# Performance work log

Hardware: AMD Instinct MI355X
Metric: run time of the kernel (lower is better)

Reference implementation:

```python
import jax, jax.numpy as jnp
import numpy as np

EMBED_DIM = 1024
NUM_HEADS = 16
HEAD_DIM = EMBED_DIM // NUM_HEADS
B, T = 4, 1024
NEG = -1.0e9
LN_EPS = 1e-5


def setup_inputs() -> dict:
    key = jax.random.key(0)
    ks = jax.random.split(key, 13)
    s = 1.0 / np.sqrt(EMBED_DIM)
    return {
        "query": jax.random.normal(ks[0], (B, T, EMBED_DIM), jnp.float32),
        "key": jax.random.normal(ks[1], (B, T, EMBED_DIM), jnp.float32),
        "value": jax.random.normal(ks[2], (B, T, EMBED_DIM), jnp.float32),
        "mask": jax.random.randint(ks[3], (B, 1, T, T), 0, 2, jnp.int32),
        "Wq": jax.random.normal(ks[4], (EMBED_DIM, EMBED_DIM), jnp.float32) * s,
        "bq": jnp.zeros((EMBED_DIM,), jnp.float32),
        "Wk": jax.random.normal(ks[5], (EMBED_DIM, EMBED_DIM), jnp.float32) * s,
        "bk": jnp.zeros((EMBED_DIM,), jnp.float32),
        "Wv": jax.random.normal(ks[6], (EMBED_DIM, EMBED_DIM), jnp.float32) * s,
        "bv": jnp.zeros((EMBED_DIM,), jnp.float32),
        "Wo": jax.random.normal(ks[7], (EMBED_DIM, EMBED_DIM), jnp.float32) * s,
        "bo": jnp.zeros((EMBED_DIM,), jnp.float32),
        "gamma": jnp.ones((EMBED_DIM,), jnp.float32),
        "beta": jnp.zeros((EMBED_DIM,), jnp.float32),
    }


def _split_heads(x):
    # (B, T, E) -> (B, H, T, D)
    b, t, _ = x.shape
    return x.reshape(b, t, NUM_HEADS, HEAD_DIM).transpose(0, 2, 1, 3)


def _mha(query, key, value, mask, Wq, bq, Wk, bk, Wv, bv, Wo, bo, gamma, beta,
         temperature=1.0):
    q = _split_heads(query @ Wq.T + bq)
    k = _split_heads(key @ Wk.T + bk)
    v = _split_heads(value @ Wv.T + bv)
    # scores: (B, H, T, T)
    scale = jnp.sqrt(jnp.float32(HEAD_DIM)) * temperature
    scores = jnp.einsum("bhqd,bhkd->bhqk", q, k) / scale
    scores = jnp.where(mask == 0, NEG, scores)
    scores = scores - jnp.max(scores, axis=-1, keepdims=True)
    # temperature >= 0.01 in this config, so the low-temperature hard-cutoff
    # branch is skipped (matches torch's Python-level `if temperature < 0.01`).
    scores = jnp.nan_to_num(scores, nan=0.0, posinf=1.0e9, neginf=-1.0e9)
    attn = jax.nn.softmax(scores, axis=-1)
    # eval mode: dropout is identity (self.training is False)
    out = jnp.einsum("bhqk,bhkd->bhqd", attn, v)  # (B, H, T, D)
    out = out.transpose(0, 2, 1, 3).reshape(query.shape[0], query.shape[1], EMBED_DIM)
    out = out @ Wo.T + bo
    # layer norm over embed_dim
    mu = jnp.mean(out, axis=-1, keepdims=True)
    var = jnp.mean(jnp.square(out - mu), axis=-1, keepdims=True)
    out = (out - mu) * jax.lax.rsqrt(var + LN_EPS) * gamma + beta
    return out


def reference(query, key, value, mask, Wq, bq, Wk, bk, Wv, bv, Wo, bo, gamma, beta):
    return _mha(query, key, value, mask, Wq, bq, Wk, bk, Wv, bv, Wo, bo, gamma, beta)
```

## Files before the change

### kernel.cpp

```cpp
#include <hip/hip_runtime.h>
#include <cmath>

#define T_SEQ 1024
#define EMB   1024
#define NH    16
#define HD    64
#define NB    4
#define BQ    64
#define BK    64

#define QSCALE 0.18033688011112042f
#define BIAS2  -1.44269504e9f

using frag8   = __attribute__((ext_vector_type(8))) short;
using f32x4   = __attribute__((ext_vector_type(4))) float;
using short4v = __attribute__((ext_vector_type(4))) short;
using short8v = __attribute__((ext_vector_type(8))) short;

__device__ inline short f2bf(float f) {
    union { float f; unsigned u; } x; x.f = f;
    unsigned r = (x.u + 0x7FFFu + ((x.u >> 16) & 1u)) >> 16;
    return (short)r;
}
__device__ inline float bf2f(unsigned short u) {
    union { unsigned u; float f; } x; x.u = ((unsigned)u) << 16;
    return x.f;
}
__device__ inline int cvt_pk_bf16(float lo, float hi) {
    int r;
    asm("v_cvt_pk_bf16_f32 %0, %1, %2" : "=v"(r) : "v"(lo), "v"(hi));
    return r;
}

__device__ inline void glds16(const short* g, short* l) {
    __builtin_amdgcn_global_load_lds(
        (const __attribute__((address_space(1))) void*)g,
        (__attribute__((address_space(3))) void*)l, 16, 0, 0);
}

struct ConvArgs { const float* src[7]; short* dst[7]; int n8[7]; };

__global__ __launch_bounds__(256) void convert_bf16(ConvArgs a) {
    const int y = blockIdx.y;
    const int t = blockIdx.x * 256 + threadIdx.x;
    if (t >= a.n8[y]) return;
    const float4* s = (const float4*)a.src[y];
    const float4 v0 = s[t * 2], v1 = s[t * 2 + 1];
    short8v o;
    o[0] = f2bf(v0.x); o[1] = f2bf(v0.y); o[2] = f2bf(v0.z); o[3] = f2bf(v0.w);
    o[4] = f2bf(v1.x); o[5] = f2bf(v1.y); o[6] = f2bf(v1.z); o[7] = f2bf(v1.w);
    *(short8v*)&a.dst[y][t * 8] = o;
}

__global__ __launch_bounds__(256) void convert_mask(
    const int* __restrict__ mask, short* __restrict__ dst)
{
    const int wave = threadIdx.x >> 6, lane = threadIdx.x & 63;
    const int tile = blockIdx.x * 4 + wave;
    const int bb   = tile >> 12;
    const int q16  = (tile >> 6) & 63;
    const int k16  = tile & 63;
    const int qrow = lane >> 2;
    const int col4 = (lane & 3) * 4;
    const int4 mv = *(const int4*)&mask[((size_t)bb * T_SEQ + q16 * 16 + qrow) * T_SEQ
                                        + k16 * 16 + col4];
    const short BB = f2bf(BIAS2);
    short4v o;
    o[0] = mv.x ? (short)0 : BB;
    o[1] = mv.y ? (short)0 : BB;
    o[2] = mv.z ? (short)0 : BB;
    o[3] = mv.w ? (short)0 : BB;
    *(short4v*)&dst[(size_t)tile * 256 + qrow * 16 + col4] = o;
}

struct GemmB { const short* A; const short* W; const float* bias; short* out; float scale; };
struct QkvArgs { GemmB g[3]; };

template <int MODE>
__device__ inline void gemm_core(short* __restrict__ As,
                                 short* __restrict__ Bs,
                                 const short* __restrict__ A,
                                 const short* __restrict__ W,
                                 const float* __restrict__ bias,
                                 float scale,
                                 short* __restrict__ outS,
                                 float* __restrict__ outF,
                                 int m0, int n0)
{
    const int tid  = threadIdx.x;
    const int wave = tid >> 6;
    const int lane = tid & 63;
    const int quad = lane >> 4;
    const int lm   = lane & 15;
    const int wr   = wave >> 1;
    const int wc   = wave & 1;
    const int K    = EMB;

    const int G0 = wave * 64 + lane, G1 = G0 + 256;
    const short* aSrc0 = A + (size_t)(m0 + (G0 >> 2)) * K + (G0 & 3) * 8;
    const short* aSrc1 = A + (size_t)(m0 + (G1 >> 2)) * K + (G1 & 3) * 8;
    const short* bSrc0 = W + (size_t)(n0 + (G0 >> 2)) * K + (G0 & 3) * 8;
    const short* bSrc1 = W + (size_t)(n0 + (G1 >> 2)) * K + (G1 & 3) * 8;
    short* aDst0 = As + wave * 512;
    short* aDst1 = As + 2048 + wave * 512;
    short* bDst0 = Bs + wave * 512;
    short* bDst1 = Bs + 2048 + wave * 512;

    f32x4 acc[4][4];
#pragma unroll
    for (int i = 0; i < 4; ++i)
#pragma unroll
        for (int j = 0; j < 4; ++j) acc[i][j] = (f32x4){0.f, 0.f, 0.f, 0.f};

    for (int kk = 0; kk < K; kk += 64) {
        __syncthreads();
        glds16(aSrc0 + kk,      aDst0);
        glds16(aSrc1 + kk,      aDst1);
        glds16(bSrc0 + kk,      bDst0);
        glds16(bSrc1 + kk,      bDst1);
        glds16(aSrc0 + kk + 32, aDst0 + 4096);
        glds16(aSrc1 + kk + 32, aDst1 + 4096);
        glds16(bSrc0 + kk + 32, bDst0 + 4096);
        glds16(bSrc1 + kk + 32, bDst1 + 4096);
        __syncthreads();

#pragma unroll
        for (int p = 0; p < 2; ++p) {
            frag8 aF[4], bF[4];
#pragma unroll
            for (int i = 0; i < 4; ++i)
                aF[i] = *(const frag8*)&As[p * 4096 + (wr * 64 + i * 16 + lm) * 32 + quad * 8];
#pragma unroll
            for (int j = 0; j < 4; ++j)
                bF[j] = *(const frag8*)&Bs[p * 4096 + (wc * 64 + j * 16 + lm) * 32 + quad * 8];
#pragma unroll
            for (int i = 0; i < 4; ++i)
#pragma unroll
                for (int j = 0; j < 4; ++j)
                    acc[i][j] = __builtin_amdgcn_mfma_f32_16x16x32_bf16(
                        aF[i], bF[j], acc[i][j], 0, 0, 0);
        }
    }

#pragma unroll
    for (int i = 0; i < 4; ++i)
#pragma unroll
        for (int j = 0; j < 4; ++j) {
            const int n = n0 + wc * 64 + j * 16 + lm;
            const float bv = bias[n];
#pragma unroll
            for (int rr = 0; rr < 4; ++rr) {
                const int m = m0 + wr * 64 + i * 16 + quad * 4 + rr;
                const float val = (acc[i][j][rr] + bv) * scale;
                if (MODE == 0) {
                    outF[((size_t)(m >> 4) * 64 + (n >> 4)) * 256 +
                         rr * 64 + quad * 16 + lm] = val;
                } else {
                    const int bb = m >> 10, tt = m & 1023;
                    const int h = n >> 6,  d  = n & 63;
                    const size_t bh = (size_t)bb * NH + h;
                    if (MODE == 1) {
                        outS[((bh * 64 + (tt >> 4)) * 8 + (d >> 3)) * 128 +
                             (tt & 15) * 8 + (d & 7)] = f2bf(val);
                    } else {
                        outS[((((bh * 16 + (tt >> 6)) * 2 + ((tt >> 5) & 1)) * 4 +
                              (d >> 4)) * 4 + ((tt >> 2) & 3)) * 128 +
                             (d & 15) * 8 + (((tt & 16) >> 2) | (tt & 3))] = f2bf(val);
                    }
                }
            }
        }
}

__global__ __launch_bounds__(256, 4) void gemm_qkv(QkvArgs args) {
    __shared__ short As[2 * 128 * 32];
    __shared__ short Bs[2 * 128 * 32];
    const int id = blockIdx.x + 8 * blockIdx.y + 256 * blockIdx.z;
    const int a  = id & 7;
    const int k2 = id >> 3;
    const int nb = k2 & 7;
    const int c  = k2 >> 3;
    const int pair = a * 12 + c;
    const int mb = pair & 31;
    const int zb = pair >> 5;
    const GemmB g = args.g[zb];
    if (zb < 2) gemm_core<1>(As, Bs, g.A, g.W, g.bias, g.scale, g.out, nullptr, mb * 128, nb * 128);
    else        gemm_core<2>(As, Bs, g.A, g.W, g.bias, g.scale, g.out, nullptr, mb * 128, nb * 128);
}

__global__ __launch_bounds__(256, 4) void gemm_wo(const short* __restrict__ A,
                                                  const short* __restrict__ W,
                                                  const float* __restrict__ bias,
                                                  float* __restrict__ out) {
    __shared__ short As[2 * 128 * 32];
    __shared__ short Bs[2 * 128 * 32];
    const int id = blockIdx.x + 8 * blockIdx.y;
    const int a  = id & 7;
    const int k2 = id >> 3;
    const int nb = k2 & 7;
    const int c  = k2 >> 3;
    const int mb = a * 4 + c;
    gemm_core<0>(As, Bs, A, W, bias, 1.0f, nullptr, out, mb * 128, nb * 128);
}

__global__ __launch_bounds__(512, 4) void flash_attn_mfma(
    const short* __restrict__ qf_, const short* __restrict__ kf_,
    const short* __restrict__ vf_, const short* __restrict__ mf_,
    short* __restrict__ out)
{
    __shared__ short KV[2][4][4096];

    const int tid  = threadIdx.x;
    const int wave = tid >> 6;
    const int lane = tid & 63;
    const int quad = lane >> 4;
    const int lm   = lane & 15;
    const int wq   = wave & 3;
    const int wk   = wave >> 2;

    const int id  = blockIdx.x;
    const int xcd = id & 7;
    const int idx = id >> 3;
    const int bh_i = xcd * 8 + (idx >> 4);
    const int b  = bh_i >> 4, h = bh_i & 15;
    const int q0 = (idx & 15) * BQ;
    const size_t bh = (size_t)bh_i;

    const int  sbuf  = wave >> 1;
    const int  shalf = (wave & 1) * 2048;
    const short* sb = ((sbuf < 2) ? kf_ : vf_) + bh * 65536
                      + (size_t)(sbuf & 1) * 32768 + shalf + lane * 8;

    const short* qb_ = qf_ + (bh * 64 + (q0 >> 4) + wq) * 1024;
    const frag8 qfa = *(const frag8*)&qb_[(quad * 16 + lm) * 8];
    const frag8 qfb = *(const frag8*)&qb_[((quad + 4) * 16 + lm) * 8];

    const short* mrow = mf_ + ((size_t)b * 64 + (q0 >> 4) + wq) * (64 * 256)
                        + lm * 16 + quad * 4;

    union { int i[4]; frag8 f; } ones;
    ones.i[0] = ones.i[1] = ones.i[2] = ones.i[3] = 0x3F803F80;

    f32x4 of[4];
#pragma unroll
    for (int dc = 0; dc < 4; ++dc) of[dc] = (f32x4){0.f, 0.f, 0.f, 0.f};
    f32x4 ls = (f32x4){0.f, 0.f, 0.f, 0.f};

#pragma unroll
    for (int it = 0; it < 4; ++it)
        glds16(sb + it * 512, &KV[0][sbuf][shalf + it * 512]);
    short4v mb[4];
#pragma unroll
    for (int kc = 0; kc < 4; ++kc)
        mb[kc] = *(const short4v*)&mrow[(wk * 32 + kc) * 256];
    __syncthreads();

    for (int kt = 0; kt < 8; ++kt) {
        const int cur = kt & 1;

        if (kt < 7) {
#pragma unroll
            for (int it = 0; it < 4; ++it)
                glds16(sb + (kt + 1) * 4096 + it * 512,
                       &KV[cur ^ 1][sbuf][shalf + it * 512]);
        }
        short4v mc[4];
#pragma unroll
        for (int kc = 0; kc < 4; ++kc) mc[kc] = mb[kc];
        if (kt < 7) {
#pragma unroll
            for (int kc = 0; kc < 4; ++kc)
                mb[kc] = *(const short4v*)&mrow[((wk * 8 + kt + 1) * 4 + kc) * 256];
        }

        f32x4 s[4];
#pragma unroll
        for (int kc = 0; kc < 4; ++kc) {
            const short* kb = &KV[cur][wk][kc * 1024];
            const frag8 kfa = *(const frag8*)&kb[(quad * 16 + lm) * 8];
            const frag8 kfb = *(const frag8*)&kb[((quad + 4) * 16 + lm) * 8];
            f32x4 a = (f32x4){ bf2f((unsigned short)mc[kc][0]),
                               bf2f((unsigned short)mc[kc][1]),
                               bf2f((unsigned short)mc[kc][2]),
                               bf2f((unsigned short)mc[kc][3]) };
            a = __builtin_amdgcn_mfma_f32_16x16x32_bf16(kfa, qfa, a, 0, 0, 0);
            a = __builtin_amdgcn_mfma_f32_16x16x32_bf16(kfb, qfb, a, 0, 0, 0);
            s[kc] = a;
        }

#pragma unroll
        for (int kc = 0; kc < 4; ++kc) {
            s[kc][0] = exp2f(s[kc][0]); s[kc][1] = exp2f(s[kc][1]);
            s[kc][2] = exp2f(s[kc][2]); s[kc][3] = exp2f(s[kc][3]);
        }

        union { int i[4]; frag8 f; } ua, ub;
        ua.i[0] = cvt_pk_bf16(s[0][0], s[0][1]);
        ua.i[1] = cvt_pk_bf16(s[0][2], s[0][3]);
        ua.i[2] = cvt_pk_bf16(s[1][0], s[1][1]);
        ua.i[3] = cvt_pk_bf16(s[1][2], s[1][3]);
        ub.i[0] = cvt_pk_bf16(s[2][0], s[2][1]);
        ub.i[1] = cvt_pk_bf16(s[2][2], s[2][3]);
        ub.i[2] = cvt_pk_bf16(s[3][0], s[3][1]);
        ub.i[3] = cvt_pk_bf16(s[3][2], s[3][3]);

        __builtin_amdgcn_s_setprio(1);
#pragma unroll
        for (int dc = 0; dc < 4; ++dc) {
            const frag8 v0 = *(const frag8*)&KV[cur][2 + wk][(dc * 4 + quad) * 128 + lm * 8];
            const frag8 v1 = *(const frag8*)&KV[cur][2 + wk][((4 + dc) * 4 + quad) * 128 + lm * 8];
            of[dc] = __builtin_amdgcn_mfma_f32_16x16x32_bf16(v0, ua.f, of[dc], 0, 0, 0);
            of[dc] = __builtin_amdgcn_mfma_f32_16x16x32_bf16(v1, ub.f, of[dc], 0, 0, 0);
        }
        ls = __builtin_amdgcn_mfma_f32_16x16x32_bf16(ones.f, ua.f, ls, 0, 0, 0);
        ls = __builtin_amdgcn_mfma_f32_16x16x32_bf16(ones.f, ub.f, ls, 0, 0, 0);
        __builtin_amdgcn_s_setprio(0);

        __syncthreads();
    }

    float* Osh = (float*)&KV[0][0][0];
    if (wk) {
#pragma unroll
        for (int c = 0; c < 16; ++c) Osh[(wq * 17 + c) * 64 + lane] = of[c >> 2][c & 3];
        Osh[(wq * 17 + 16) * 64 + lane] = ls[0];
    }
    __syncthreads();
    if (!wk) {
#pragma unroll
        for (int c = 0; c < 16; ++c) of[c >> 2][c & 3] += Osh[(wq * 17 + c) * 64 + lane];
        const float lsum = ls[0] + Osh[(wq * 17 + 16) * 64 + lane];
        const float inv = 1.0f / lsum;

        short* ob = out + ((size_t)b * T_SEQ + q0 + wq * 16 + lm) * EMB + h * HD;
#pragma unroll
        for (int dc = 0; dc < 4; ++dc) {
            short4v o4;
#pragma unroll
            for (int rr = 0; rr < 4; ++rr) o4[rr] = f2bf(of[dc][rr] * inv);
            *(short4v*)&ob[dc * 16 + quad * 4] = o4;
        }
    }
}

__global__ __launch_bounds__(256) void layernorm_k(
    const float* __restrict__ x, const float* __restrict__ gamma,
    const float* __restrict__ beta, float* __restrict__ out)
{
    __shared__ float ws1[4], ws2[4];
    const int tid = threadIdx.x;
    const int row = blockIdx.x;
    const int m16 = row >> 4, rr = row & 3, qd = (row >> 2) & 3;

    const float4 v = *(const float4*)&x[((size_t)m16 * 64 + (tid >> 2)) * 256 +
                                        rr * 64 + qd * 16 + (tid & 3) * 4];
    float s  = v.x + v.y + v.z + v.w;
    float ss = v.x * v.x + v.y * v.y + v.z * v.z + v.w * v.w;
#pragma unroll
    for (int off = 32; off > 0; off >>= 1) {
        s  += __shfl_down(s, off);
        ss += __shfl_down(ss, off);
    }
    if ((tid & 63) == 0) { ws1[tid >> 6] = s; ws2[tid >> 6] = ss; }
    __syncthreads();
    if (tid == 0) {
        const float a = ws1[0] + ws1[1] + ws1[2] + ws1[3];
        const float bsum = ws2[0] + ws2[1] + ws2[2] + ws2[3];
        const float mu = a * (1.0f / EMB);
        const float var = bsum * (1.0f / EMB) - mu * mu;
        ws1[0] = mu;
        ws2[0] = rsqrtf(var + 1e-5f);
    }
    __syncthreads();
    const float mu = ws1[0], rstd = ws2[0];

    const float4 g = *(const float4*)&gamma[tid * 4];
    const float4 bt = *(const float4*)&beta[tid * 4];
    float4 r;
    r.x = (v.x - mu) * rstd * g.x + bt.x;
    r.y = (v.y - mu) * rstd * g.y + bt.y;
    r.z = (v.z - mu) * rstd * g.z + bt.z;
    r.w = (v.w - mu) * rstd * g.w + bt.w;
    *(float4*)&out[(size_t)row * EMB + tid * 4] = r;
}

extern "C" void kernel_launch(void* const* d_in, const int* in_sizes, int n_in,
                              void* d_out, int out_size, void* d_ws, size_t ws_size,
                              hipStream_t stream) {
    const float* query = (const float*)d_in[0];
    const float* key_i = (const float*)d_in[1];
    const float* value = (const float*)d_in[2];
    const int*   mask  = (const int*)d_in[3];
    const float* Wq = (const float*)d_in[4];
    const float* bq = (const float*)d_in[5];
    const float* Wk = (const float*)d_in[6];
    const float* bk = (const float*)d_in[7];
    const float* Wv = (const float*)d_in[8];
    const float* bv = (const float*)d_in[9];
    const float* Wo = (const float*)d_in[10];
    const float* bo = (const float*)d_in[11];
    const float* gamma = (const float*)d_in[12];
    const float* beta  = (const float*)d_in[13];

    const size_t SZ = (size_t)NB * T_SEQ * EMB;
    const size_t WZ = (size_t)EMB * EMB;
    short* sws = (short*)d_ws;
    short* q_bf  = sws;
    short* k_bf  = sws + SZ;
    short* v_bf  = sws + 2 * SZ;
    short* w_bf  = sws + 3 * SZ;
    short* qh    = sws + 4 * SZ;
    short* kh    = sws + 5 * SZ;
    short* vh    = sws + 6 * SZ;
    short* maskb = sws + 7 * SZ;
    short* attnb = q_bf;
    float* projb = (float*)(sws + SZ);

    ConvArgs ca;
    ca.src[0] = query; ca.dst[0] = q_bf;          ca.n8[0] = (int)(SZ / 8);
    ca.src[1] = key_i; ca.dst[1] = k_bf;          ca.n8[1] = (int)(SZ / 8);
    ca.src[2] = value; ca.dst[2] = v_bf;          ca.n8[2] = (int)(SZ / 8);
    ca.src[3] = Wq;    ca.dst[3] = w_bf;          ca.n8[3] = (int)(WZ / 8);
    ca.src[4] = Wk;    ca.dst[4] = w_bf + WZ;     ca.n8[4] = (int)(WZ / 8);
    ca.src[5] = Wv;    ca.dst[5] = w_bf + 2 * WZ; ca.n8[5] = (int)(WZ / 8);
    ca.src[6] = Wo;    ca.dst[6] = w_bf + 3 * WZ; ca.n8[6] = (int)(WZ / 8);
    convert_bf16<<<dim3((SZ / 8 + 255) / 256, 7), 256, 0, stream>>>(ca);

    convert_mask<<<dim3(NB * 64 * 64 / 4), 256, 0, stream>>>(mask, maskb);

    QkvArgs qa;
    qa.g[0] = { q_bf, w_bf,          bq, qh, QSCALE };
    qa.g[1] = { k_bf, w_bf + WZ,     bk, kh, 1.0f };
    qa.g[2] = { v_bf, w_bf + 2 * WZ, bv, vh, 1.0f };
    gemm_qkv<<<dim3(EMB / 128, NB * T_SEQ / 128, 3), 256, 0, stream>>>(qa);

    flash_attn_mfma<<<dim3(T_SEQ / BQ * NH * NB), 512, 0, stream>>>(qh, kh, vh, maskb, attnb);

    gemm_wo<<<dim3(EMB / 128, NB * T_SEQ / 128), 256, 0, stream>>>(
        attnb, w_bf + 3 * WZ, bo, projb);

    layernorm_k<<<dim3(NB * T_SEQ), 256, 0, stream>>>(projb, gamma, beta, (float*)d_out);
}
```

Measured before the change: 244.1 us.

## Split Wo GEMM along K and restructure flash attention to 128-row query tiles

Flash attention now gives each of its 8 waves its own 16-row query slice over the full key range, with a 128-row query block. This removes the cross-wave split-K reduction through shared memory and halves the KV LDS footprint, but halves the block count. The Wo projection is split into two K-halves written to separate fp32 buffers, doubling its grid to improve occupancy. Layernorm sums the two partials, which adds an extra fp32 read of the projection output.

```diff
diff --git a/kernel.cpp b/kernel.cpp
--- a/kernel.cpp
+++ b/kernel.cpp
@@ -6,7 +6,7 @@
 #define NH    16
 #define HD    64
 #define NB    4
-#define BQ    64
+#define BQ    128
 #define BK    64
 
 #define QSCALE 0.18033688011112042f
@@ -85,7 +85,7 @@
                                  float scale,
                                  short* __restrict__ outS,
                                  float* __restrict__ outF,
-                                 int m0, int n0)
+                                 int m0, int n0, int k0, int kspan)
 {
     const int tid  = threadIdx.x;
     const int wave = tid >> 6;
@@ -112,7 +112,7 @@
 #pragma unroll
         for (int j = 0; j < 4; ++j) acc[i][j] = (f32x4){0.f, 0.f, 0.f, 0.f};
 
-    for (int kk = 0; kk < K; kk += 64) {
+    for (int kk = k0; kk < k0 + kspan; kk += 64) {
         __syncthreads();
         glds16(aSrc0 + kk,      aDst0);
         glds16(aSrc1 + kk,      aDst1);
@@ -147,7 +147,7 @@
 #pragma unroll
         for (int j = 0; j < 4; ++j) {
             const int n = n0 + wc * 64 + j * 16 + lm;
-            const float bv = bias[n];
+            const float bv = (k0 == 0) ? bias[n] : 0.0f;
 #pragma unroll
             for (int rr = 0; rr < 4; ++rr) {
                 const int m = m0 + wr * 64 + i * 16 + quad * 4 + rr;
@@ -184,23 +184,28 @@
     const int mb = pair & 31;
     const int zb = pair >> 5;
     const GemmB g = args.g[zb];
-    if (zb < 2) gemm_core<1>(As, Bs, g.A, g.W, g.bias, g.scale, g.out, nullptr, mb * 128, nb * 128);
-    else        gemm_core<2>(As, Bs, g.A, g.W, g.bias, g.scale, g.out, nullptr, mb * 128, nb * 128);
+    if (zb < 2) gemm_core<1>(As, Bs, g.A, g.W, g.bias, g.scale, g.out, nullptr,
+                             mb * 128, nb * 128, 0, EMB);
+    else        gemm_core<2>(As, Bs, g.A, g.W, g.bias, g.scale, g.out, nullptr,
+                             mb * 128, nb * 128, 0, EMB);
 }
 
 __global__ __launch_bounds__(256, 4) void gemm_wo(const short* __restrict__ A,
                                                   const short* __restrict__ W,
                                                   const float* __restrict__ bias,
-                                                  float* __restrict__ out) {
+                                                  float* __restrict__ out0,
+                                                  float* __restrict__ out1) {
     __shared__ short As[2 * 128 * 32];
     __shared__ short Bs[2 * 128 * 32];
     const int id = blockIdx.x + 8 * blockIdx.y;
     const int a  = id & 7;
-    const int k2 = id >> 3;
-    const int nb = k2 & 7;
-    const int c  = k2 >> 3;
-    const int mb = a * 4 + c;
-    gemm_core<0>(As, Bs, A, W, bias, 1.0f, nullptr, out, mb * 128, nb * 128);
+    const int r  = id >> 3;
+    const int nb = r & 7;
+    const int pr = a * 8 + (r >> 3);
+    const int mb = pr & 31;
+    const int ks = pr >> 5;
+    gemm_core<0>(As, Bs, A, W, bias, 1.0f, nullptr, ks ? out1 : out0,
+                 mb * 128, nb * 128, ks * 512, 512);
 }
 
 __global__ __launch_bounds__(512, 4) void flash_attn_mfma(
@@ -208,34 +213,32 @@
     const short* __restrict__ vf_, const short* __restrict__ mf_,
     short* __restrict__ out)
 {
-    __shared__ short KV[2][4][4096];
+    __shared__ short KV[2][2][4096];
 
     const int tid  = threadIdx.x;
     const int wave = tid >> 6;
     const int lane = tid & 63;
     const int quad = lane >> 4;
     const int lm   = lane & 15;
-    const int wq   = wave & 3;
-    const int wk   = wave >> 2;
 
     const int id  = blockIdx.x;
     const int xcd = id & 7;
     const int idx = id >> 3;
-    const int bh_i = xcd * 8 + (idx >> 4);
+    const int bh_i = xcd * 8 + (idx >> 3);
     const int b  = bh_i >> 4, h = bh_i & 15;
-    const int q0 = (idx & 15) * BQ;
+    const int qb = idx & 7;
+    const int q0 = qb * BQ;
     const size_t bh = (size_t)bh_i;
 
-    const int  sbuf  = wave >> 1;
-    const int  shalf = (wave & 1) * 2048;
-    const short* sb = ((sbuf < 2) ? kf_ : vf_) + bh * 65536
-                      + (size_t)(sbuf & 1) * 32768 + shalf + lane * 8;
-
-    const short* qb_ = qf_ + (bh * 64 + (q0 >> 4) + wq) * 1024;
+    const short* sbase = ((wave < 4) ? kf_ : vf_) + bh * 65536
+                         + (wave & 3) * 1024 + lane * 8;
+    short* dstb = &KV[0][0][0] + (wave >> 2) * 4096 + (wave & 3) * 1024;
+
+    const short* qb_ = qf_ + (bh * 64 + qb * 8 + wave) * 1024;
     const frag8 qfa = *(const frag8*)&qb_[(quad * 16 + lm) * 8];
     const frag8 qfb = *(const frag8*)&qb_[((quad + 4) * 16 + lm) * 8];
 
-    const short* mrow = mf_ + ((size_t)b * 64 + (q0 >> 4) + wq) * (64 * 256)
+    const short* mrow = mf_ + ((size_t)b * 64 + qb * 8 + wave) * (64 * 256)
                         + lm * 16 + quad * 4;
 
     union { int i[4]; frag8 f; } ones;
@@ -246,37 +249,35 @@
     for (int dc = 0; dc < 4; ++dc) of[dc] = (f32x4){0.f, 0.f, 0.f, 0.f};
     f32x4 ls = (f32x4){0.f, 0.f, 0.f, 0.f};
 
-#pragma unroll
-    for (int it = 0; it < 4; ++it)
-        glds16(sb + it * 512, &KV[0][sbuf][shalf + it * 512]);
+    glds16(sbase,       dstb);
+    glds16(sbase + 512, dstb + 512);
     short4v mb[4];
 #pragma unroll
     for (int kc = 0; kc < 4; ++kc)
-        mb[kc] = *(const short4v*)&mrow[(wk * 32 + kc) * 256];
+        mb[kc] = *(const short4v*)&mrow[kc * 256];
     __syncthreads();
 
-    for (int kt = 0; kt < 8; ++kt) {
+    for (int kt = 0; kt < 16; ++kt) {
         const int cur = kt & 1;
 
-        if (kt < 7) {
-#pragma unroll
-            for (int it = 0; it < 4; ++it)
-                glds16(sb + (kt + 1) * 4096 + it * 512,
-                       &KV[cur ^ 1][sbuf][shalf + it * 512]);
+        if (kt < 15) {
+            short* nd = dstb + (cur ^ 1) * 8192;
+            glds16(sbase + (kt + 1) * 4096,       nd);
+            glds16(sbase + (kt + 1) * 4096 + 512, nd + 512);
         }
         short4v mc[4];
 #pragma unroll
         for (int kc = 0; kc < 4; ++kc) mc[kc] = mb[kc];
-        if (kt < 7) {
+        if (kt < 15) {
 #pragma unroll
             for (int kc = 0; kc < 4; ++kc)
-                mb[kc] = *(const short4v*)&mrow[((wk * 8 + kt + 1) * 4 + kc) * 256];
+                mb[kc] = *(const short4v*)&mrow[((kt + 1) * 4 + kc) * 256];
         }
 
         f32x4 s[4];
 #pragma unroll
         for (int kc = 0; kc < 4; ++kc) {
-            const short* kb = &KV[cur][wk][kc * 1024];
+            const short* kb = &KV[cur][0][kc * 1024];
             const frag8 kfa = *(const frag8*)&kb[(quad * 16 + lm) * 8];
             const frag8 kfb = *(const frag8*)&kb[((quad + 4) * 16 + lm) * 8];
             f32x4 a = (f32x4){ bf2f((unsigned short)mc[kc][0]),
@@ -307,8 +308,8 @@
         __builtin_amdgcn_s_setprio(1);
 #pragma unroll
         for (int dc = 0; dc < 4; ++dc) {
-            const frag8 v0 = *(const frag8*)&KV[cur][2 + wk][(dc * 4 + quad) * 128 + lm * 8];
-            const frag8 v1 = *(const frag8*)&KV[cur][2 + wk][((4 + dc) * 4 + quad) * 128 + lm * 8];
+            const frag8 v0 = *(const frag8*)&KV[cur][1][(dc * 4 + quad) * 128 + lm * 8];
+            const frag8 v1 = *(const frag8*)&KV[cur][1][((4 + dc) * 4 + quad) * 128 + lm * 8];
             of[dc] = __builtin_amdgcn_mfma_f32_16x16x32_bf16(v0, ua.f, of[dc], 0, 0, 0);
             of[dc] = __builtin_amdgcn_mfma_f32_16x16x32_bf16(v1, ub.f, of[dc], 0, 0, 0);
         }
@@ -319,41 +320,36 @@
         __syncthreads();
     }
 
-    float* Osh = (float*)&KV[0][0][0];
-    if (wk) {
-#pragma unroll
-        for (int c = 0; c < 16; ++c) Osh[(wq * 17 + c) * 64 + lane] = of[c >> 2][c & 3];
-        Osh[(wq * 17 + 16) * 64 + lane] = ls[0];
+    const float inv = 1.0f / ls[0];
+
+    short* ob = out + ((size_t)b * T_SEQ + q0 + wave * 16 + lm) * EMB + h * HD;
+#pragma unroll
+    for (int dc = 0; dc < 4; ++dc) {
+        short4v o4;
+#pragma unroll
+        for (int rr = 0; rr < 4; ++rr) o4[rr] = f2bf(of[dc][rr] * inv);
+        *(short4v*)&ob[dc * 16 + quad * 4] = o4;
     }
-    __syncthreads();
-    if (!wk) {
-#pragma unroll
-        for (int c = 0; c < 16; ++c) of[c >> 2][c & 3] += Osh[(wq * 17 + c) * 64 + lane];
-        const float lsum = ls[0] + Osh[(wq * 17 + 16) * 64 + lane];
-        const float inv = 1.0f / lsum;
-
-        short* ob = out + ((size_t)b * T_SEQ + q0 + wq * 16 + lm) * EMB + h * HD;
-#pragma unroll
-        for (int dc = 0; dc < 4; ++dc) {
-            short4v o4;
-#pragma unroll
-            for (int rr = 0; rr < 4; ++rr) o4[rr] = f2bf(of[dc][rr] * inv);
-            *(short4v*)&ob[dc * 16 + quad * 4] = o4;
-        }
-    }
 }
 
 __global__ __launch_bounds__(256) void layernorm_k(
-    const float* __restrict__ x, const float* __restrict__ gamma,
-    const float* __restrict__ beta, float* __restrict__ out)
+    const float* __restrict__ x0, const float* __restrict__ x1,
+    const float* __restrict__ gamma, const float* __restrict__ beta,
+    float* __restrict__ out)
 {
     __shared__ float ws1[4], ws2[4];
     const int tid = threadIdx.x;
     const int row = blockIdx.x;
     const int m16 = row >> 4, rr = row & 3, qd = (row >> 2) & 3;
 
-    const float4 v = *(const float4*)&x[((size_t)m16 * 64 + (tid >> 2)) * 256 +
-                                        rr * 64 + qd * 16 + (tid & 3) * 4];
+    const size_t ix = ((size_t)m16 * 64 + (tid >> 2)) * 256 +
+                      rr * 64 + qd * 16 + (tid & 3) * 4;
+    const float4 v1 = *(const float4*)&x0[ix];
+    const float4 v2 = *(const float4*)&x1[ix];
+    float4 v;
+    v.x = v1.x + v2.x; v.y = v1.y + v2.y;
+    v.z = v1.z + v2.z; v.w = v1.w + v2.w;
+
     float s  = v.x + v.y + v.z + v.w;
     float ss = v.x * v.x + v.y * v.y + v.z * v.z + v.w * v.w;
 #pragma unroll
@@ -414,7 +410,8 @@
     short* vh    = sws + 6 * SZ;
     short* maskb = sws + 7 * SZ;
     short* attnb = q_bf;
-    float* projb = (float*)(sws + SZ);
+    float* projb  = (float*)(sws + SZ);
+    float* projb2 = (float*)(sws + 4 * SZ);
 
     ConvArgs ca;
     ca.src[0] = query; ca.dst[0] = q_bf;          ca.n8[0] = (int)(SZ / 8);
@@ -436,8 +433,7 @@
 
     flash_attn_mfma<<<dim3(T_SEQ / BQ * NH * NB), 512, 0, stream>>>(qh, kh, vh, maskb, attnb);
 
-    gemm_wo<<<dim3(EMB / 128, NB * T_SEQ / 128), 256, 0, stream>>>(
-        attnb, w_bf + 3 * WZ, bo, projb);
-
-    layernorm_k<<<dim3(NB * T_SEQ), 256, 0, stream>>>(projb, gamma, beta, (float*)d_out);
-}
+    gemm_wo<<<dim3(8, 64), 256, 0, stream>>>(attnb, w_bf + 3 * WZ, bo, projb, projb2);
+
+    layernorm_k<<<dim3(NB * T_SEQ), 256, 0, stream>>>(projb, projb2, gamma, beta, (float*)d_out);
+}
```

Result: faster. 233.1 us (-4.5%).
